# Performance work log

Measured on AMD Instinct MI355X. Metric: run time of the kernel, lower is better.

The kernel has to match this reference:

```python
import jax, jax.numpy as jnp
import numpy as np

IGNORE_INDEX = 255


def setup_inputs() -> dict:
    key = jax.random.key(0)
    k1, k2 = jax.random.split(key)
    n, h, w = 8, 256, 256
    num_class, cnum = 20, 4
    c = num_class * cnum
    P = 8192  # number of parcel segments
    features = jax.random.normal(k1, (n, c, h, w), dtype=jnp.float32)
    parcel = jax.random.randint(k2, (n, h, w), 0, P, dtype=jnp.int32)
    # all pixels of a parcel share one class label (as the torch code assumes)
    target = (parcel % num_class).astype(jnp.int32)
    return {"features": features, "target": target, "parcel": parcel,
            "num_segments": P, "cnum": cnum, "num_class": num_class}


def reference(features, target, parcel, num_segments, cnum, num_class):
    n, c, h, w = features.shape
    hw = h * w
    # n c h w -> n (h w) c
    fea = features.reshape(n, c, hw).transpose(0, 2, 1)
    # MaxPool1d(cnum, stride=cnum) over channel dim: group consecutive cnum channels
    branch_dis = fea.reshape(n, hw, num_class, cnum).max(axis=-1)  # [n, hw, num_class]
    branch_dis = branch_dis.reshape(n * hw, num_class)

    t = target.reshape(-1)
    p = parcel.reshape(-1)
    valid = t != IGNORE_INDEX
    wgt = valid.astype(branch_dis.dtype)

    # fused segment-mean replacing the python loop over unique parcel ids
    seg_sum = jax.ops.segment_sum(branch_dis * wgt[:, None], p, num_segments=num_segments)
    counts = jax.ops.segment_sum(wgt, p, num_segments=num_segments)
    seg_mean = seg_sum / jnp.maximum(counts, 1.0)[:, None]  # [P, num_class]

    # per-parcel target (labels are constant within a parcel -> max == first)
    t_masked = jnp.where(valid, t, -1)
    tgt_parcel = jax.ops.segment_max(t_masked, p, num_segments=num_segments)
    seg_valid = (counts > 0).astype(seg_mean.dtype)

    logp = jax.nn.log_softmax(seg_mean, axis=-1)
    tgt_safe = jnp.clip(tgt_parcel, 0, num_class - 1)
    nll = -jnp.take_along_axis(logp, tgt_safe[:, None], axis=1)[:, 0]
    loss_dis = jnp.sum(nll * seg_valid) / jnp.maximum(jnp.sum(seg_valid), 1.0)

    # diversity branch: softmax over spatial dim, channel-group maxpool
    branch_div = jax.nn.softmax(fea, axis=1)  # softmax over hw
    branch_div = branch_div.reshape(n, hw, num_class, cnum).max(axis=-1)
    loss_div = 1.0 - jnp.mean(jnp.sum(branch_div, axis=1)) / num_class
    return loss_dis, loss_div
```

## Files before the change

kernel.cpp:

```cpp
#include <hip/hip_runtime.h>
#include <float.h>

#define IGNORE_INDEX 255

constexpr int N_IMG = 8;
constexpr int C     = 80;
constexpr int HW    = 65536;
constexpr int NC    = 20;
constexpr int CNUM  = 4;
constexpr int P     = 8192;
constexpr int NPIX  = N_IMG * HW;
constexpr int STRIPES = 4;
constexpr int NCH   = N_IMG * C;

constexpr size_t B_BD    = 0;
constexpr size_t B_SORT  = (size_t)NPIX * 20 * 4;
constexpr size_t B_CNT   = B_SORT + (size_t)NPIX * 4;
constexpr size_t B_ACC   = B_CNT + (size_t)P * 4;
constexpr size_t B_OFF   = B_ACC + 64;
constexpr size_t B_WOFF  = B_OFF + (size_t)P * 4;
constexpr size_t B_PM    = B_WOFF + (size_t)P * 4;
constexpr size_t B_PS    = B_PM + (size_t)NCH * STRIPES * 4;
constexpr size_t B_CHOFF = B_PS + (size_t)NCH * STRIPES * 4;
constexpr size_t NEED    = B_CHOFF + (size_t)NCH * 4;

__device__ __forceinline__ float waveMax(float v) {
#pragma unroll
  for (int o = 32; o > 0; o >>= 1) v = fmaxf(v, __shfl_down(v, o, 64));
  return v;
}
__device__ __forceinline__ float waveSum(float v) {
#pragma unroll
  for (int o = 32; o > 0; o >>= 1) v += __shfl_down(v, o, 64);
  return v;
}


__global__ __launch_bounds__(256) void stats_kernel(
    const float* __restrict__ f, float* __restrict__ pm, float* __restrict__ ps) {
  const int ch = blockIdx.x >> 2, stripe = blockIdx.x & 3;
  const float4* base =
      (const float4*)(f + (size_t)ch * HW + (size_t)stripe * (HW / STRIPES));
  const int n4 = HW / STRIPES / 4;
  float m = -FLT_MAX;
  for (int i = threadIdx.x; i < n4; i += 256) {
    float4 v = base[i];
    m = fmaxf(m, fmaxf(fmaxf(v.x, v.y), fmaxf(v.z, v.w)));
  }
  __shared__ float sred[4];
  __shared__ float bcast;
  const int wid = threadIdx.x >> 6, lid = threadIdx.x & 63;
  float wm = waveMax(m);
  if (lid == 0) sred[wid] = wm;
  __syncthreads();
  if (threadIdx.x == 0)
    bcast = fmaxf(fmaxf(sred[0], sred[1]), fmaxf(sred[2], sred[3]));
  __syncthreads();
  const float M = bcast;
  float s = 0.f;
  for (int i = threadIdx.x; i < n4; i += 256) {
    float4 v = base[i];
    s += __expf(v.x - M) + __expf(v.y - M) + __expf(v.z - M) + __expf(v.w - M);
  }
  float wsv = waveSum(s);
  __syncthreads();
  if (lid == 0) sred[wid] = wsv;
  __syncthreads();
  if (threadIdx.x == 0) {
    pm[blockIdx.x] = M;
    ps[blockIdx.x] = sred[0] + sred[1] + sred[2] + sred[3];
  }
}

__global__ void combine_kernel(const float* __restrict__ pm,
                               const float* __restrict__ ps,
                               float* __restrict__ choff) {
  const int ch = threadIdx.x;
  if (ch >= NCH) return;
  float m = -FLT_MAX;
#pragma unroll
  for (int i = 0; i < STRIPES; i++) m = fmaxf(m, pm[ch * STRIPES + i]);
  float s = 0.f;
#pragma unroll
  for (int i = 0; i < STRIPES; i++)
    s += ps[ch * STRIPES + i] * __expf(pm[ch * STRIPES + i] - m);
  choff[ch] = m + logf(s);
}

__global__ __launch_bounds__(256) void hist_kernel(
    const int* __restrict__ target, const int* __restrict__ parcel,
    int* __restrict__ cnt) {
  const int t4 = blockIdx.x * 256 + threadIdx.x;
  const int4 tv = ((const int4*)target)[t4];
  const int4 pv = ((const int4*)parcel)[t4];
  if (tv.x != IGNORE_INDEX) atomicAdd(&cnt[pv.x], 1);
  if (tv.y != IGNORE_INDEX) atomicAdd(&cnt[pv.y], 1);
  if (tv.z != IGNORE_INDEX) atomicAdd(&cnt[pv.z], 1);
  if (tv.w != IGNORE_INDEX) atomicAdd(&cnt[pv.w], 1);
}

__global__ __launch_bounds__(1024) void scan_kernel(
    const int* __restrict__ cnt, int* __restrict__ offs, int* __restrict__ woff) {
  __shared__ int sh[1024];
  const int t = threadIdx.x;
  const int4* c4 = (const int4*)(cnt + t * 8);
  int4 a = c4[0], b = c4[1];
  int c[8] = {a.x, a.y, a.z, a.w, b.x, b.y, b.z, b.w};
  int tot = 0;
#pragma unroll
  for (int j = 0; j < 8; j++) tot += c[j];
  sh[t] = tot;
  __syncthreads();
  for (int d = 1; d < 1024; d <<= 1) {
    int v = (t >= d) ? sh[t - d] : 0;
    __syncthreads();
    sh[t] += v;
    __syncthreads();
  }
  int e = sh[t] - tot;
#pragma unroll
  for (int j = 0; j < 8; j++) {
    offs[t * 8 + j] = e;
    woff[t * 8 + j] = e;
    e += c[j];
  }
}

__global__ __launch_bounds__(256) void scatter_kernel(
    const int* __restrict__ target, const int* __restrict__ parcel,
    int* __restrict__ woff, unsigned* __restrict__ sorted) {
  const int t4 = blockIdx.x * 256 + threadIdx.x;
  const int4 tv = ((const int4*)target)[t4];
  const int4 pv = ((const int4*)parcel)[t4];
  const int pix0 = t4 * 4;
  int tarr[4] = {tv.x, tv.y, tv.z, tv.w};
  int parr[4] = {pv.x, pv.y, pv.z, pv.w};
#pragma unroll
  for (int i = 0; i < 4; i++) {
    if (tarr[i] != IGNORE_INDEX) {
      int pos = atomicAdd(&woff[parr[i]], 1);
      sorted[pos] = ((unsigned)tarr[i] << 19) | (unsigned)(pix0 + i);
    }
  }
}

__global__ __launch_bounds__(256) void divbd_kernel(
    const float* __restrict__ f, const float* __restrict__ choff,
    float* __restrict__ bd, float* __restrict__ div_acc) {
  const int pg = blockIdx.x * 256 + threadIdx.x;
  const int img = blockIdx.x >> 8;
  const int pix = pg & (HW - 1);
  const float* fb = f + (size_t)img * C * HW + pix;
  __shared__ float soff[C];
  if (threadIdx.x < C) soff[threadIdx.x] = choff[img * C + threadIdx.x];
  __syncthreads();
  float dm[NC];
  float divs = 0.f;
#pragma unroll
  for (int k = 0; k < NC; k++) {
    float d = -FLT_MAX, e = -FLT_MAX;
#pragma unroll
    for (int j = 0; j < CNUM; j++) {
      const int ch = k * CNUM + j;
      float v = fb[(size_t)ch * HW];
      d = fmaxf(d, v);
      e = fmaxf(e, v - soff[ch]);
    }
    dm[k] = d;
    divs += __expf(e);
  }
  float4* o = (float4*)(bd + (size_t)pg * NC);
  o[0] = make_float4(dm[0], dm[1], dm[2], dm[3]);
  o[1] = make_float4(dm[4], dm[5], dm[6], dm[7]);
  o[2] = make_float4(dm[8], dm[9], dm[10], dm[11]);
  o[3] = make_float4(dm[12], dm[13], dm[14], dm[15]);
  o[4] = make_float4(dm[16], dm[17], dm[18], dm[19]);

  __shared__ float sred[4];
  const int wid = threadIdx.x >> 6, lid = threadIdx.x & 63;
  float wsum = waveSum(divs);
  if (lid == 0) sred[wid] = wsum;
  __syncthreads();
  if (threadIdx.x == 0)
    atomicAdd(div_acc, sred[0] + sred[1] + sred[2] + sred[3]);
}

__global__ __launch_bounds__(256) void parcel_kernel(
    const float* __restrict__ bd, const unsigned* __restrict__ sorted,
    const int* __restrict__ cnt, const int* __restrict__ offs,
    float* __restrict__ acc) {
  const int wid = threadIdx.x >> 6, lid = threadIdx.x & 63;
  const int p = blockIdx.x * 4 + wid;
  const int c = cnt[p];
  float sums[NC];
#pragma unroll
  for (int k = 0; k < NC; k++) sums[k] = 0.f;
  int tmax = -1;
  if (c > 0) {
    const int start = offs[p];
    for (int i = lid; i < c; i += 64) {
      const unsigned u = sorted[start + i];
      const int pix = (int)(u & 524287u);
      tmax = max(tmax, (int)(u >> 19));
      const float4* b = (const float4*)(bd + (size_t)pix * NC);
      float4 b0 = b[0], b1 = b[1], b2 = b[2], b3 = b[3], b4 = b[4];
      sums[0] += b0.x;  sums[1] += b0.y;  sums[2] += b0.z;  sums[3] += b0.w;
      sums[4] += b1.x;  sums[5] += b1.y;  sums[6] += b1.z;  sums[7] += b1.w;
      sums[8] += b2.x;  sums[9] += b2.y;  sums[10] += b2.z; sums[11] += b2.w;
      sums[12] += b3.x; sums[13] += b3.y; sums[14] += b3.z; sums[15] += b3.w;
      sums[16] += b4.x; sums[17] += b4.y; sums[18] += b4.z; sums[19] += b4.w;
    }
  }
#pragma unroll
  for (int o = 32; o > 0; o >>= 1) {
#pragma unroll
    for (int k = 0; k < NC; k++) sums[k] += __shfl_xor(sums[k], o, 64);
    tmax = max(tmax, __shfl_xor(tmax, o, 64));
  }
  float nll = 0.f, val = 0.f;
  if (c > 0) {
    const float inv = 1.f / (float)c;
    float mean[NC];
    float m = -FLT_MAX;
#pragma unroll
    for (int k = 0; k < NC; k++) {
      mean[k] = sums[k] * inv;
      m = fmaxf(m, mean[k]);
    }
    float se = 0.f;
#pragma unroll
    for (int k = 0; k < NC; k++) se += __expf(mean[k] - m);
    const float lse = m + logf(se);
    const int t = min(max(tmax, 0), NC - 1);
    nll = lse - mean[t];
    val = 1.f;
  }
  __shared__ float sn[4], sv[4];
  if (lid == 0) { sn[wid] = nll; sv[wid] = val; }
  __syncthreads();
  if (threadIdx.x == 0) {
    atomicAdd(&acc[1], sn[0] + sn[1] + sn[2] + sn[3]);
    atomicAdd(&acc[2], sv[0] + sv[1] + sv[2] + sv[3]);
  }
}

__global__ void finalize_kernel(const float* __restrict__ acc,
                                float* __restrict__ out) {
  out[0] = acc[1] / fmaxf(acc[2], 1.f);
  out[1] = 1.f - acc[0] / (float)(N_IMG * NC * NC);
}

constexpr size_t OFF_SEGSUM = 0;
constexpr size_t OFF_COUNTS = 163840;
constexpr size_t OFF_CHOFF  = 172032;
constexpr size_t OFF_ACC    = 172672;
constexpr size_t BYTE_TGT   = 690752;
constexpr size_t BYTE_ZERO  = 690752;
constexpr size_t BYTE_TGT_N = P * sizeof(int);

__global__ __launch_bounds__(256) void chan_stats_fb(
    const float* __restrict__ f, float* __restrict__ chan_off) {
  const int ch = blockIdx.x;
  const float4* base = (const float4*)(f + (size_t)ch * HW);
  const int n4 = HW / 4;
  float m = -FLT_MAX;
  for (int i = threadIdx.x; i < n4; i += 256) {
    float4 v = base[i];
    m = fmaxf(m, fmaxf(fmaxf(v.x, v.y), fmaxf(v.z, v.w)));
  }
  __shared__ float sred[4];
  __shared__ float bcast;
  const int wid = threadIdx.x >> 6, lid = threadIdx.x & 63;
  float wm = waveMax(m);
  if (lid == 0) sred[wid] = wm;
  __syncthreads();
  if (threadIdx.x == 0)
    bcast = fmaxf(fmaxf(sred[0], sred[1]), fmaxf(sred[2], sred[3]));
  __syncthreads();
  const float M = bcast;
  float s = 0.f;
  for (int i = threadIdx.x; i < n4; i += 256) {
    float4 v = base[i];
    s += __expf(v.x - M) + __expf(v.y - M) + __expf(v.z - M) + __expf(v.w - M);
  }
  float wsv = waveSum(s);
  __syncthreads();
  if (lid == 0) sred[wid] = wsv;
  __syncthreads();
  if (threadIdx.x == 0)
    chan_off[ch] = M + logf(sred[0] + sred[1] + sred[2] + sred[3]);
}

__global__ __launch_bounds__(256) void pixel_fb(
    const float* __restrict__ f, const int* __restrict__ target,
    const int* __restrict__ parcel, const float* __restrict__ chan_off,
    float* __restrict__ seg_sum, float* __restrict__ counts,
    int* __restrict__ tgtp, float* __restrict__ div_acc) {
  const int t4 = blockIdx.x * 256 + threadIdx.x;
  const int img = t4 / (HW / 4);
  const int pix0 = (t4 % (HW / 4)) * 4;
  const float* fb = f + (size_t)img * C * HW;
  __shared__ float soff[C];
  if (threadIdx.x < C) soff[threadIdx.x] = chan_off[img * C + threadIdx.x];
  __syncthreads();
  const int4 tv = *(const int4*)(target + (size_t)img * HW + pix0);
  const int4 pv = *(const int4*)(parcel + (size_t)img * HW + pix0);
  int tarr[4] = {tv.x, tv.y, tv.z, tv.w};
  int parr[4] = {pv.x, pv.y, pv.z, pv.w};
  bool val[4];
#pragma unroll
  for (int i = 0; i < 4; i++) val[i] = (tarr[i] != IGNORE_INDEX);
  float divs = 0.f;
#pragma unroll
  for (int k = 0; k < NC; k++) {
    float4 dmax = make_float4(-FLT_MAX, -FLT_MAX, -FLT_MAX, -FLT_MAX);
    float4 em = make_float4(-FLT_MAX, -FLT_MAX, -FLT_MAX, -FLT_MAX);
#pragma unroll
    for (int j = 0; j < CNUM; j++) {
      const int ch = k * CNUM + j;
      float4 v = *(const float4*)(fb + (size_t)ch * HW + pix0);
      const float off = soff[ch];
      dmax.x = fmaxf(dmax.x, v.x); dmax.y = fmaxf(dmax.y, v.y);
      dmax.z = fmaxf(dmax.z, v.z); dmax.w = fmaxf(dmax.w, v.w);
      em.x = fmaxf(em.x, v.x - off); em.y = fmaxf(em.y, v.y - off);
      em.z = fmaxf(em.z, v.z - off); em.w = fmaxf(em.w, v.w - off);
    }
    divs += __expf(em.x) + __expf(em.y) + __expf(em.z) + __expf(em.w);
    float dmv[4] = {dmax.x, dmax.y, dmax.z, dmax.w};
#pragma unroll
    for (int i = 0; i < 4; i++)
      if (val[i]) atomicAdd(&seg_sum[parr[i] * NC + k], dmv[i]);
  }
#pragma unroll
  for (int i = 0; i < 4; i++) {
    if (val[i]) {
      atomicAdd(&counts[parr[i]], 1.0f);
      atomicMax(&tgtp[parr[i]], tarr[i]);
    }
  }
  __shared__ float sred[4];
  const int wid = threadIdx.x >> 6, lid = threadIdx.x & 63;
  float wsum = waveSum(divs);
  if (lid == 0) sred[wid] = wsum;
  __syncthreads();
  if (threadIdx.x == 0)
    atomicAdd(div_acc, sred[0] + sred[1] + sred[2] + sred[3]);
}

__global__ __launch_bounds__(256) void seg_fb(
    const float* __restrict__ seg_sum, const float* __restrict__ counts,
    const int* __restrict__ tgtp, float* __restrict__ nll_acc,
    float* __restrict__ vcnt_acc) {
  const int s = blockIdx.x * 256 + threadIdx.x;
  const float cntv = counts[s];
  const float valid = (cntv > 0.f) ? 1.f : 0.f;
  const float inv = 1.f / fmaxf(cntv, 1.f);
  float mean[NC];
  float m = -FLT_MAX;
#pragma unroll
  for (int k = 0; k < NC; k++) {
    mean[k] = seg_sum[s * NC + k] * inv;
    m = fmaxf(m, mean[k]);
  }
  float se = 0.f;
#pragma unroll
  for (int k = 0; k < NC; k++) se += __expf(mean[k] - m);
  const float lse = m + logf(se);
  int t = tgtp[s];
  t = min(max(t, 0), NC - 1);
  const float nll = (lse - mean[t]) * valid;
  __shared__ float sn[4], sv[4];
  const int wid = threadIdx.x >> 6, lid = threadIdx.x & 63;
  float wn = waveSum(nll);
  float wv = waveSum(valid);
  if (lid == 0) { sn[wid] = wn; sv[wid] = wv; }
  __syncthreads();
  if (threadIdx.x == 0) {
    atomicAdd(nll_acc, sn[0] + sn[1] + sn[2] + sn[3]);
    atomicAdd(vcnt_acc, sv[0] + sv[1] + sv[2] + sv[3]);
  }
}

extern "C" void kernel_launch(void* const* d_in, const int* in_sizes, int n_in,
                              void* d_out, int out_size, void* d_ws,
                              size_t ws_size, hipStream_t stream) {
  const float* features = (const float*)d_in[0];
  const int*   target   = (const int*)d_in[1];
  const int*   parcel   = (const int*)d_in[2];
  float* out = (float*)d_out;
  char* wsb = (char*)d_ws;

  if (ws_size >= NEED) {
    float*    bd     = (float*)(wsb + B_BD);
    unsigned* sorted = (unsigned*)(wsb + B_SORT);
    int*      cnt    = (int*)(wsb + B_CNT);
    float*    acc    = (float*)(wsb + B_ACC);
    int*      offs   = (int*)(wsb + B_OFF);
    int*      woff   = (int*)(wsb + B_WOFF);
    float*    pm     = (float*)(wsb + B_PM);
    float*    ps     = (float*)(wsb + B_PS);
    float*    choff  = (float*)(wsb + B_CHOFF);

    hipMemsetAsync(wsb + B_CNT, 0, P * 4 + 64, stream);

    stats_kernel<<<NCH * STRIPES, 256, 0, stream>>>(features, pm, ps);
    combine_kernel<<<1, 640, 0, stream>>>(pm, ps, choff);
    hist_kernel<<<NPIX / 4 / 256, 256, 0, stream>>>(target, parcel, cnt);
    scan_kernel<<<1, 1024, 0, stream>>>(cnt, offs, woff);
    scatter_kernel<<<NPIX / 4 / 256, 256, 0, stream>>>(target, parcel, woff,
                                                       sorted);
    divbd_kernel<<<NPIX / 256, 256, 0, stream>>>(features, choff, bd, acc + 0);
    parcel_kernel<<<P / 4, 256, 0, stream>>>(bd, sorted, cnt, offs, acc);
    finalize_kernel<<<1, 1, 0, stream>>>(acc, out);
  } else {
    float* ws       = (float*)d_ws;
    float* seg_sum  = ws + OFF_SEGSUM;
    float* counts   = ws + OFF_COUNTS;
    float* chan_off = ws + OFF_CHOFF;
    float* acc      = ws + OFF_ACC;
    int*   tgtp     = (int*)(wsb + BYTE_TGT);

    hipMemsetAsync(d_ws, 0, BYTE_ZERO, stream);
    hipMemsetAsync(wsb + BYTE_TGT, 0xFF, BYTE_TGT_N, stream);
    chan_stats_fb<<<NCH, 256, 0, stream>>>(features, chan_off);
    pixel_fb<<<NPIX / 4 / 256, 256, 0, stream>>>(features, target, parcel,
                                                 chan_off, seg_sum, counts,
                                                 tgtp, acc + 0);
    seg_fb<<<P / 256, 256, 0, stream>>>(seg_sum, counts, tgtp, acc + 1,
                                        acc + 2);
    finalize_kernel<<<1, 1, 0, stream>>>(acc, out);
  }
}
```

Before: 411.4 us.

## Scatter branch_dis rows directly into parcel-sorted order and fuse small kernels

```diff
diff --git a/kernel.cpp b/kernel.cpp
--- a/kernel.cpp
+++ b/kernel.cpp
@@ -13,16 +13,16 @@
 constexpr int STRIPES = 4;
 constexpr int NCH   = N_IMG * C;
 
-constexpr size_t B_BD    = 0;
-constexpr size_t B_SORT  = (size_t)NPIX * 20 * 4;
-constexpr size_t B_CNT   = B_SORT + (size_t)NPIX * 4;
+constexpr size_t B_BDS   = 0;
+constexpr size_t B_CNT   = (size_t)NPIX * 20 * 4;
 constexpr size_t B_ACC   = B_CNT + (size_t)P * 4;
 constexpr size_t B_OFF   = B_ACC + 64;
 constexpr size_t B_WOFF  = B_OFF + (size_t)P * 4;
 constexpr size_t B_PM    = B_WOFF + (size_t)P * 4;
 constexpr size_t B_PS    = B_PM + (size_t)NCH * STRIPES * 4;
 constexpr size_t B_CHOFF = B_PS + (size_t)NCH * STRIPES * 4;
-constexpr size_t NEED    = B_CHOFF + (size_t)NCH * 4;
+constexpr size_t B_TGT   = B_CHOFF + (size_t)NCH * 4;
+constexpr size_t NEED    = B_TGT + (size_t)P * 4;
 
 __device__ __forceinline__ float waveMax(float v) {
 #pragma unroll
@@ -35,9 +35,20 @@
   return v;
 }
 
-
-__global__ __launch_bounds__(256) void stats_kernel(
-    const float* __restrict__ f, float* __restrict__ pm, float* __restrict__ ps) {
+__global__ __launch_bounds__(256) void stats_hist_kernel(
+    const float* __restrict__ f, const int* __restrict__ target,
+    const int* __restrict__ parcel, float* __restrict__ pm,
+    float* __restrict__ ps, int* __restrict__ cnt) {
+  if (blockIdx.x >= NCH * STRIPES) {
+    const int t4 = (blockIdx.x - NCH * STRIPES) * 256 + threadIdx.x;
+    const int4 tv = ((const int4*)target)[t4];
+    const int4 pv = ((const int4*)parcel)[t4];
+    if (tv.x != IGNORE_INDEX) atomicAdd(&cnt[pv.x], 1);
+    if (tv.y != IGNORE_INDEX) atomicAdd(&cnt[pv.y], 1);
+    if (tv.z != IGNORE_INDEX) atomicAdd(&cnt[pv.z], 1);
+    if (tv.w != IGNORE_INDEX) atomicAdd(&cnt[pv.w], 1);
+    return;
+  }
   const int ch = blockIdx.x >> 2, stripe = blockIdx.x & 3;
   const float4* base =
       (const float4*)(f + (size_t)ch * HW + (size_t)stripe * (HW / STRIPES));
@@ -72,37 +83,22 @@
   }
 }
 
-__global__ void combine_kernel(const float* __restrict__ pm,
-                               const float* __restrict__ ps,
-                               float* __restrict__ choff) {
-  const int ch = threadIdx.x;
-  if (ch >= NCH) return;
-  float m = -FLT_MAX;
-#pragma unroll
-  for (int i = 0; i < STRIPES; i++) m = fmaxf(m, pm[ch * STRIPES + i]);
-  float s = 0.f;
-#pragma unroll
-  for (int i = 0; i < STRIPES; i++)
-    s += ps[ch * STRIPES + i] * __expf(pm[ch * STRIPES + i] - m);
-  choff[ch] = m + logf(s);
-}
-
-__global__ __launch_bounds__(256) void hist_kernel(
-    const int* __restrict__ target, const int* __restrict__ parcel,
-    int* __restrict__ cnt) {
-  const int t4 = blockIdx.x * 256 + threadIdx.x;
-  const int4 tv = ((const int4*)target)[t4];
-  const int4 pv = ((const int4*)parcel)[t4];
-  if (tv.x != IGNORE_INDEX) atomicAdd(&cnt[pv.x], 1);
-  if (tv.y != IGNORE_INDEX) atomicAdd(&cnt[pv.y], 1);
-  if (tv.z != IGNORE_INDEX) atomicAdd(&cnt[pv.z], 1);
-  if (tv.w != IGNORE_INDEX) atomicAdd(&cnt[pv.w], 1);
-}
-
-__global__ __launch_bounds__(1024) void scan_kernel(
-    const int* __restrict__ cnt, int* __restrict__ offs, int* __restrict__ woff) {
+__global__ __launch_bounds__(1024) void combine_scan_kernel(
+    const float* __restrict__ pm, const float* __restrict__ ps,
+    float* __restrict__ choff, const int* __restrict__ cnt,
+    int* __restrict__ offs, int* __restrict__ woff) {
+  const int t = threadIdx.x;
+  if (t < NCH) {
+    float m = -FLT_MAX;
+#pragma unroll
+    for (int i = 0; i < STRIPES; i++) m = fmaxf(m, pm[t * STRIPES + i]);
+    float s = 0.f;
+#pragma unroll
+    for (int i = 0; i < STRIPES; i++)
+      s += ps[t * STRIPES + i] * __expf(pm[t * STRIPES + i] - m);
+    choff[t] = m + logf(s);
+  }
   __shared__ int sh[1024];
-  const int t = threadIdx.x;
   const int4* c4 = (const int4*)(cnt + t * 8);
   int4 a = c4[0], b = c4[1];
   int c[8] = {a.x, a.y, a.z, a.w, b.x, b.y, b.z, b.w};
@@ -126,29 +122,13 @@
   }
 }
 
-__global__ __launch_bounds__(256) void scatter_kernel(
-    const int* __restrict__ target, const int* __restrict__ parcel,
-    int* __restrict__ woff, unsigned* __restrict__ sorted) {
-  const int t4 = blockIdx.x * 256 + threadIdx.x;
-  const int4 tv = ((const int4*)target)[t4];
-  const int4 pv = ((const int4*)parcel)[t4];
-  const int pix0 = t4 * 4;
-  int tarr[4] = {tv.x, tv.y, tv.z, tv.w};
-  int parr[4] = {pv.x, pv.y, pv.z, pv.w};
-#pragma unroll
-  for (int i = 0; i < 4; i++) {
-    if (tarr[i] != IGNORE_INDEX) {
-      int pos = atomicAdd(&woff[parr[i]], 1);
-      sorted[pos] = ((unsigned)tarr[i] << 19) | (unsigned)(pix0 + i);
-    }
-  }
-}
-
-__global__ __launch_bounds__(256) void divbd_kernel(
-    const float* __restrict__ f, const float* __restrict__ choff,
-    float* __restrict__ bd, float* __restrict__ div_acc) {
+__global__ __launch_bounds__(256) void divbd_scatter_kernel(
+    const float* __restrict__ f, const int* __restrict__ target,
+    const int* __restrict__ parcel, const float* __restrict__ choff,
+    int* __restrict__ woff, float* __restrict__ bds, int* __restrict__ tgtp,
+    float* __restrict__ div_acc) {
   const int pg = blockIdx.x * 256 + threadIdx.x;
-  const int img = blockIdx.x >> 8;
+  const int img = pg >> 16;
   const int pix = pg & (HW - 1);
   const float* fb = f + (size_t)img * C * HW + pix;
   __shared__ float soff[C];
@@ -169,13 +149,18 @@
     dm[k] = d;
     divs += __expf(e);
   }
-  float4* o = (float4*)(bd + (size_t)pg * NC);
-  o[0] = make_float4(dm[0], dm[1], dm[2], dm[3]);
-  o[1] = make_float4(dm[4], dm[5], dm[6], dm[7]);
-  o[2] = make_float4(dm[8], dm[9], dm[10], dm[11]);
-  o[3] = make_float4(dm[12], dm[13], dm[14], dm[15]);
-  o[4] = make_float4(dm[16], dm[17], dm[18], dm[19]);
-
+  const int t = target[pg];
+  const int p = parcel[pg];
+  if (t != IGNORE_INDEX) {
+    const int pos = atomicAdd(&woff[p], 1);
+    float4* o = (float4*)(bds + (size_t)pos * NC);
+    o[0] = make_float4(dm[0], dm[1], dm[2], dm[3]);
+    o[1] = make_float4(dm[4], dm[5], dm[6], dm[7]);
+    o[2] = make_float4(dm[8], dm[9], dm[10], dm[11]);
+    o[3] = make_float4(dm[12], dm[13], dm[14], dm[15]);
+    o[4] = make_float4(dm[16], dm[17], dm[18], dm[19]);
+    tgtp[p] = t;
+  }
   __shared__ float sred[4];
   const int wid = threadIdx.x >> 6, lid = threadIdx.x & 63;
   float wsum = waveSum(divs);
@@ -186,8 +171,8 @@
 }
 
 __global__ __launch_bounds__(256) void parcel_kernel(
-    const float* __restrict__ bd, const unsigned* __restrict__ sorted,
-    const int* __restrict__ cnt, const int* __restrict__ offs,
+    const float* __restrict__ bds, const int* __restrict__ cnt,
+    const int* __restrict__ offs, const int* __restrict__ tgtp,
     float* __restrict__ acc) {
   const int wid = threadIdx.x >> 6, lid = threadIdx.x & 63;
   const int p = blockIdx.x * 4 + wid;
@@ -195,14 +180,10 @@
   float sums[NC];
 #pragma unroll
   for (int k = 0; k < NC; k++) sums[k] = 0.f;
-  int tmax = -1;
   if (c > 0) {
     const int start = offs[p];
     for (int i = lid; i < c; i += 64) {
-      const unsigned u = sorted[start + i];
-      const int pix = (int)(u & 524287u);
-      tmax = max(tmax, (int)(u >> 19));
-      const float4* b = (const float4*)(bd + (size_t)pix * NC);
+      const float4* b = (const float4*)(bds + (size_t)(start + i) * NC);
       float4 b0 = b[0], b1 = b[1], b2 = b[2], b3 = b[3], b4 = b[4];
       sums[0] += b0.x;  sums[1] += b0.y;  sums[2] += b0.z;  sums[3] += b0.w;
       sums[4] += b1.x;  sums[5] += b1.y;  sums[6] += b1.z;  sums[7] += b1.w;
@@ -215,7 +196,6 @@
   for (int o = 32; o > 0; o >>= 1) {
 #pragma unroll
     for (int k = 0; k < NC; k++) sums[k] += __shfl_xor(sums[k], o, 64);
-    tmax = max(tmax, __shfl_xor(tmax, o, 64));
   }
   float nll = 0.f, val = 0.f;
   if (c > 0) {
@@ -231,7 +211,7 @@
 #pragma unroll
     for (int k = 0; k < NC; k++) se += __expf(mean[k] - m);
     const float lse = m + logf(se);
-    const int t = min(max(tmax, 0), NC - 1);
+    const int t = min(max(tgtp[p], 0), NC - 1);
     nll = lse - mean[t];
     val = 1.f;
   }
@@ -391,26 +371,25 @@
   char* wsb = (char*)d_ws;
 
   if (ws_size >= NEED) {
-    float*    bd     = (float*)(wsb + B_BD);
-    unsigned* sorted = (unsigned*)(wsb + B_SORT);
-    int*      cnt    = (int*)(wsb + B_CNT);
-    float*    acc    = (float*)(wsb + B_ACC);
-    int*      offs   = (int*)(wsb + B_OFF);
-    int*      woff   = (int*)(wsb + B_WOFF);
-    float*    pm     = (float*)(wsb + B_PM);
-    float*    ps     = (float*)(wsb + B_PS);
-    float*    choff  = (float*)(wsb + B_CHOFF);
+    float* bds   = (float*)(wsb + B_BDS);
+    int*   cnt   = (int*)(wsb + B_CNT);
+    float* acc   = (float*)(wsb + B_ACC);
+    int*   offs  = (int*)(wsb + B_OFF);
+    int*   woff  = (int*)(wsb + B_WOFF);
+    float* pm    = (float*)(wsb + B_PM);
+    float* ps    = (float*)(wsb + B_PS);
+    float* choff = (float*)(wsb + B_CHOFF);
+    int*   tgtp  = (int*)(wsb + B_TGT);
 
     hipMemsetAsync(wsb + B_CNT, 0, P * 4 + 64, stream);
 
-    stats_kernel<<<NCH * STRIPES, 256, 0, stream>>>(features, pm, ps);
-    combine_kernel<<<1, 640, 0, stream>>>(pm, ps, choff);
-    hist_kernel<<<NPIX / 4 / 256, 256, 0, stream>>>(target, parcel, cnt);
-    scan_kernel<<<1, 1024, 0, stream>>>(cnt, offs, woff);
-    scatter_kernel<<<NPIX / 4 / 256, 256, 0, stream>>>(target, parcel, woff,
-                                                       sorted);
-    divbd_kernel<<<NPIX / 256, 256, 0, stream>>>(features, choff, bd, acc + 0);
-    parcel_kernel<<<P / 4, 256, 0, stream>>>(bd, sorted, cnt, offs, acc);
+    stats_hist_kernel<<<NCH * STRIPES + NPIX / 1024, 256, 0, stream>>>(
+        features, target, parcel, pm, ps, cnt);
+    combine_scan_kernel<<<1, 1024, 0, stream>>>(pm, ps, choff, cnt, offs,
+                                                woff);
+    divbd_scatter_kernel<<<NPIX / 256, 256, 0, stream>>>(
+        features, target, parcel, choff, woff, bds, tgtp, acc + 0);
+    parcel_kernel<<<P / 4, 256, 0, stream>>>(bds, cnt, offs, tgtp, acc);
     finalize_kernel<<<1, 1, 0, stream>>>(acc, out);
   } else {
     float* ws       = (float*)d_ws;
```

New measurement: 382.9 us. 6.9% less time.
